# Optimization experiments

Measured on AMD Instinct MI355X. Metric: run time of the kernel, lower is better.

## Reference

```python
import jax, jax.numpy as jnp
import numpy as np

B = 4096           # batch
F = 16             # categorical fields
V = 50000          # vocab per field
D = 128            # embed_dim
T = 2              # task_num
ES = 8             # specific_expert_num
ESH = 8            # shared_expert_num
NUMN = 63          # numerical_num
IN0 = (F + 1) * D  # 2176 = embed_output_dim
H0, H1 = 512, 256  # bottom_mlp_dims
INV = float(1.0 / np.sqrt(1.0 + 1e-5))  # eval BatchNorm1d: running_mean=0, running_var=1


def setup_inputs():
    keys = iter(jax.random.split(jax.random.key(0), 64))
    def nrm(shape, s=0.02):
        return jax.random.normal(next(keys), shape, jnp.float32) * s
    inp = {}
    inp["categorical_x"] = jax.random.randint(next(keys), (B, F), 0, V)
    inp["numerical_x"] = jax.random.normal(next(keys), (B, NUMN), jnp.float32)
    inp["emb_table"] = nrm((F * V, D))
    inp["num_W"] = nrm((NUMN, D)); inp["num_b"] = jnp.zeros((D,), jnp.float32)
    def mlp(prefix, lead, i, o):
        inp[prefix + "_W"] = nrm(lead + (i, o))
        inp[prefix + "_b"] = jnp.zeros(lead + (o,), jnp.float32)
        inp[prefix + "_g"] = jnp.ones(lead + (o,), jnp.float32)    # BN gamma
        inp[prefix + "_be"] = jnp.zeros(lead + (o,), jnp.float32)  # BN beta
    # PLE layer 0 (input dim IN0 -> H0)
    mlp("se0", (ESH,), IN0, H0); mlp("te0", (T, ES), IN0, H0)
    inp["tg0_W"] = nrm((T, IN0, ES + ESH)); inp["tg0_b"] = jnp.zeros((T, ES + ESH), jnp.float32)
    inp["sg0_W"] = nrm((IN0, T * ES + ESH)); inp["sg0_b"] = jnp.zeros((T * ES + ESH,), jnp.float32)
    # PLE layer 1 (H0 -> H1); share gate of last layer is unused in torch forward
    mlp("se1", (ESH,), H0, H1); mlp("te1", (T, ES), H0, H1)
    inp["tg1_W"] = nrm((T, H0, ES + ESH)); inp["tg1_b"] = jnp.zeros((T, ES + ESH), jnp.float32)
    # per-task towers: [H1->128]->BN->ReLU, [128->64]->BN->ReLU, [64->1]
    mlp("tw0", (T,), H1, 128); mlp("tw1", (T,), 128, 64)
    inp["two_W"] = nrm((T, 64, 1)); inp["two_b"] = jnp.zeros((T, 1), jnp.float32)
    return inp


def _ple_layer(shared, tfea, seW, seb, seg, sebe, teW, teb, teg, tebe, tgW, tgb, sgW=None, sgb=None):
    # shared: [B, in]; tfea: [T, B, in]
    nT, nB = tfea.shape[0], tfea.shape[1]
    # shared experts: [B, ESH, o]
    sh = jax.nn.relu((jnp.einsum('bi,eio->beo', shared, seW) + seb) * INV * seg + sebe)
    # task-specific experts: [T, B, ES, o]
    th = jnp.einsum('tbi,teio->tbeo', tfea, teW) + teb[:, None]
    th = jax.nn.relu(th * INV * teg[:, None] + tebe[:, None])
    # per-task gates over [own ES experts ++ shared ESH experts]
    gate = jax.nn.softmax(jnp.einsum('tbi,tig->tbg', tfea, tgW) + tgb[:, None], axis=-1)
    mix = jnp.concatenate([th, jnp.broadcast_to(sh[None], (nT,) + sh.shape)], axis=2)
    new_t = jnp.einsum('tbg,tbgo->tbo', gate, mix)
    if sgW is None:  # last layer: shared branch not updated
        return None, new_t
    # shared gate over [all tasks' experts (task order) ++ shared experts]
    all_mix = jnp.concatenate(
        [jnp.transpose(th, (1, 0, 2, 3)).reshape(nB, nT * th.shape[2], th.shape[3]), sh], axis=1)
    g2 = jax.nn.softmax(shared @ sgW + sgb, axis=-1)
    new_s = jnp.einsum('bg,bgo->bo', g2, all_mix)
    return new_s, new_t


def reference(categorical_x, numerical_x, emb_table, num_W, num_b,
              se0_W, se0_b, se0_g, se0_be, te0_W, te0_b, te0_g, te0_be, tg0_W, tg0_b, sg0_W, sg0_b,
              se1_W, se1_b, se1_g, se1_be, te1_W, te1_b, te1_g, te1_be, tg1_W, tg1_b,
              tw0_W, tw0_b, tw0_g, tw0_be, tw1_W, tw1_b, tw1_g, tw1_be, two_W, two_b):
    offsets = jnp.arange(F) * V
    cat_emb = emb_table[categorical_x + offsets]                         # [B,F,D]
    num_emb = numerical_x @ num_W + num_b                                # [B,D]
    emb = jnp.concatenate([cat_emb.reshape(B, F * D), num_emb], axis=1)  # [B,IN0]
    shared = emb
    tfea = jnp.broadcast_to(emb[None], (T, B, IN0))
    shared, tfea = _ple_layer(shared, tfea, se0_W, se0_b, se0_g, se0_be,
                              te0_W, te0_b, te0_g, te0_be, tg0_W, tg0_b, sg0_W, sg0_b)
    _, tfea = _ple_layer(shared, tfea, se1_W, se1_b, se1_g, se1_be,
                         te1_W, te1_b, te1_g, te1_be, tg1_W, tg1_b)
    # towers (eval BN, dropout identity)
    h = jax.nn.relu((jnp.einsum('tbi,tio->tbo', tfea, tw0_W) + tw0_b[:, None]) * INV * tw0_g[:, None] + tw0_be[:, None])
    h = jax.nn.relu((jnp.einsum('tbi,tio->tbo', h, tw1_W) + tw1_b[:, None]) * INV * tw1_g[:, None] + tw1_be[:, None])
    out = jnp.einsum('tbi,tio->tbo', h, two_W) + two_b[:, None]          # [T,B,1]
    return jax.nn.sigmoid(out[..., 0])                                   # [T,B]
```

## Files before the change

kernel.cpp:

```cpp
#include <hip/hip_runtime.h>

typedef unsigned short u16;
typedef unsigned int u32;
typedef __attribute__((ext_vector_type(4))) u16 u16x4;
typedef __attribute__((ext_vector_type(8))) __bf16 bf16x8;
typedef __attribute__((ext_vector_type(4))) float floatx4;

#define INV_BN 0.9999950000374997f
#define IN0 2176
#define N0EXT 12416
#define N1EXT 2176

__device__ __forceinline__ float b2f(u16 u) {
  return __builtin_bit_cast(float, (u32)u << 16);
}
__device__ __forceinline__ u16 f2b(float f) {
  u32 x = __builtin_bit_cast(u32, f);
  return (u16)((x + 0x7fffu + ((x >> 16) & 1u)) >> 16);
}

__global__ __launch_bounds__(256) void input_build(
    const int* __restrict__ cat, const float* __restrict__ table,
    const float* __restrict__ xn, const float* __restrict__ W,
    const float* __restrict__ bias, u16* __restrict__ X0) {
  int x = blockIdx.x, tid = threadIdx.x;
  if (x < 8192) {
    int idx = x * 256 + tid;
    int d4 = idx & 31;
    int bf = idx >> 5;
    int f = bf & 15;
    int b = bf >> 4;
    long row = (long)cat[bf] + (long)f * 50000;
    float4 v = *((const float4*)(table + row * 128) + d4);
    u16x4 o = {f2b(v.x), f2b(v.y), f2b(v.z), f2b(v.w)};
    *(u16x4*)(X0 + (long)b * IN0 + f * 128 + d4 * 4) = o;
  } else {
    int idx = (x - 8192) * 256 + tid;
    int o = idx & 127;
    int b = idx >> 7;
    float acc = bias[o];
    const float* xr = xn + b * 63;
    for (int k = 0; k < 63; k++) acc = fmaf(xr[k], W[k * 128 + o], acc);
    X0[(long)b * IN0 + 2048 + o] = f2b(acc);
  }
}

__global__ __launch_bounds__(256) void repack_w_all(
    const float* __restrict__ te0W, const float* __restrict__ te0g,
    const float* __restrict__ se0W, const float* __restrict__ se0g,
    const float* __restrict__ te1W, const float* __restrict__ te1g,
    const float* __restrict__ se1W, const float* __restrict__ se1g,
    const float* __restrict__ tw0W, const float* __restrict__ tw0g,
    u16* __restrict__ W0, u16* __restrict__ W1, u16* __restrict__ TW0) {
  int z = blockIdx.z;
  const float *src, *gsc;
  u16* dst;
  int K, O, nBase, e, xm, ym;
  if (z < 16) {
    e = z; src = te0W; gsc = te0g; dst = W0; K = 2176; O = 512; nBase = 0; xm = 68; ym = 16;
  } else if (z < 24) {
    e = z - 16; src = se0W; gsc = se0g; dst = W0; K = 2176; O = 512; nBase = 8192; xm = 68; ym = 16;
  } else if (z < 40) {
    e = z - 24; src = te1W; gsc = te1g; dst = W1; K = 512; O = 256;
    nBase = (e < 8) ? 0 : (N1EXT - 2048); xm = 16; ym = 8;
  } else if (z < 48) {
    e = z - 40; src = se1W; gsc = se1g; dst = W1; K = 512; O = 256; nBase = 2 * N1EXT; xm = 16; ym = 8;
  } else {
    e = z - 48; src = tw0W; gsc = tw0g; dst = TW0; K = 256; O = 128; nBase = 0; xm = 8; ym = 4;
  }
  if (blockIdx.x >= (u32)xm || blockIdx.y >= (u32)ym) return;
  __shared__ float tile[32][33];
  int k0 = blockIdx.x * 32, o0 = blockIdx.y * 32;
  int tx = threadIdx.x & 31, ty = threadIdx.x >> 5;
  const float* S = src + (long)e * K * O;
#pragma unroll
  for (int r = 0; r < 32; r += 8)
    tile[ty + r][tx] = S[(long)(k0 + ty + r) * O + o0 + tx];
  __syncthreads();
#pragma unroll
  for (int r = 0; r < 32; r += 8) {
    int o = o0 + ty + r;
    float s = INV_BN * gsc[e * O + o];
    dst[(long)(nBase + e * O + o) * K + k0 + tx] = f2b(tile[tx][ty + r] * s);
  }
}

__global__ __launch_bounds__(256) void setup_small(
    const float* __restrict__ tg0W, const float* __restrict__ tg0b,
    const float* __restrict__ sg0W, const float* __restrict__ sg0b,
    const float* __restrict__ tg1W, const float* __restrict__ tg1b,
    const float* __restrict__ te0b, const float* __restrict__ te0g, const float* __restrict__ te0be,
    const float* __restrict__ se0b, const float* __restrict__ se0g, const float* __restrict__ se0be,
    const float* __restrict__ te1b, const float* __restrict__ te1g, const float* __restrict__ te1be,
    const float* __restrict__ se1b, const float* __restrict__ se1g, const float* __restrict__ se1be,
    const float* __restrict__ tw0b, const float* __restrict__ tw0g, const float* __restrict__ tw0be,
    const float* __restrict__ tw1W, const float* __restrict__ tw1b,
    const float* __restrict__ tw1g, const float* __restrict__ tw1be,
    u16* __restrict__ W0, u16* __restrict__ W1, u16* __restrict__ TW1,
    float* __restrict__ bias0, float* __restrict__ bias1,
    float* __restrict__ biasT0, float* __restrict__ biasT1) {
  int x = blockIdx.x, tid = threadIdx.x;
  if (x < 128) {
    int g = x;
    u16* dst = W0 + (long)(12288 + g) * IN0;
    for (int k = tid; k < IN0; k += 256) {
      float v;
      if (g < 32) {
        int t = g >> 4, j = g & 15;
        v = tg0W[(long)t * IN0 * 16 + k * 16 + j];
      } else if (g < 56) {
        v = sg0W[k * 24 + (g - 32)];
      } else {
        v = 0.f;
      }
      dst[k] = f2b(v);
    }
    if (tid == 0)
      bias0[12288 + g] = g < 32 ? tg0b[g] : (g < 56 ? sg0b[g - 32] : 0.f);
  } else if (x < 512) {
    int i = x - 128;
    int z = i >> 7, g = i & 127;
    u16* dst = W1 + (long)z * N1EXT * 512 + (long)(2048 + g) * 512;
    for (int k = tid; k < 512; k += 256) {
      float v = (z < 2 && g < 16) ? tg1W[(long)z * 512 * 16 + k * 16 + g] : 0.f;
      dst[k] = f2b(v);
    }
    if (tid == 0)
      bias1[z * N1EXT + 2048 + g] = (z < 2 && g < 16) ? tg1b[z * 16 + g] : 0.f;
  } else if (x < 640) {
    int idx = (x - 512) * 256 + tid;
    int z = idx >> 14, rem = idx & 16383, n = rem >> 7, k = rem & 127;
    float v = 0.f;
    if (n < 64) v = tw1W[(long)z * 128 * 64 + k * 64 + n] * INV_BN * tw1g[z * 64 + n];
    TW1[(long)z * 128 * 128 + n * 128 + k] = f2b(v);
    if (k == 0)
      biasT1[z * 128 + n] =
          (n < 64) ? tw1b[z * 64 + n] * INV_BN * tw1g[z * 64 + n] + tw1be[z * 64 + n] : 0.f;
  } else if (x < 688) {
    int i = (x - 640) * 256 + tid;
    if (i < 8192) bias0[i] = te0b[i] * INV_BN * te0g[i] + te0be[i];
    else {
      int r = i - 8192;
      bias0[i] = se0b[r] * INV_BN * se0g[r] + se0be[r];
    }
  } else if (x < 712) {
    int j = (x - 688) * 256 + tid;
    int z = j >> 11, r = j & 2047;
    float v;
    if (z < 2) v = te1b[z * 2048 + r] * INV_BN * te1g[z * 2048 + r] + te1be[z * 2048 + r];
    else v = se1b[r] * INV_BN * se1g[r] + se1be[r];
    bias1[z * N1EXT + r] = v;
  } else {
    biasT0[tid] = tw0b[tid] * INV_BN * tw0g[tid] + tw0be[tid];
  }
}

__device__ __forceinline__ void gemm_body(
    const u16* __restrict__ A, const u16* __restrict__ Bw, u16* __restrict__ C,
    const float* __restrict__ bias, int N, int K, int reluN, int yOff) {
  __shared__ u16 As[128 * 32];
  __shared__ u16 Bs[128 * 32];
  int tid = threadIdx.x;
  int m0 = blockIdx.x * 128, n0 = (blockIdx.y + yOff) * 128;
  int l = tid & 63, w = tid >> 6;
  int wm = (w >> 1) * 64, wn = (w & 1) * 64;

  const u16* aS0 = A + (long)(m0 + (tid >> 2)) * K + (tid & 3) * 8;
  const u16* aS1 = A + (long)(m0 + 64 + (tid >> 2)) * K + (tid & 3) * 8;
  const u16* bS0 = Bw + (long)(n0 + (tid >> 2)) * K + (tid & 3) * 8;
  const u16* bS1 = Bw + (long)(n0 + 64 + (tid >> 2)) * K + (tid & 3) * 8;
  u16* aD0 = As + tid * 8;
  u16* aD1 = As + (256 + tid) * 8;
  u16* bD0 = Bs + tid * 8;
  u16* bD1 = Bs + (256 + tid) * 8;

  floatx4 acc[4][4] = {};

  int aOff[4], bOff[4];
#pragma unroll
  for (int i = 0; i < 4; i++) {
    aOff[i] = (wm + i * 16 + (l & 15)) * 32 + (l >> 4) * 8;
    bOff[i] = (wn + i * 16 + (l & 15)) * 32 + (l >> 4) * 8;
  }

  for (int k0 = 0; k0 < K; k0 += 32) {
    __builtin_amdgcn_global_load_lds((const __attribute__((address_space(1))) u16*)aS0,
                                     (__attribute__((address_space(3))) u16*)aD0, 16, 0, 0);
    __builtin_amdgcn_global_load_lds((const __attribute__((address_space(1))) u16*)aS1,
                                     (__attribute__((address_space(3))) u16*)aD1, 16, 0, 0);
    __builtin_amdgcn_global_load_lds((const __attribute__((address_space(1))) u16*)bS0,
                                     (__attribute__((address_space(3))) u16*)bD0, 16, 0, 0);
    __builtin_amdgcn_global_load_lds((const __attribute__((address_space(1))) u16*)bS1,
                                     (__attribute__((address_space(3))) u16*)bD1, 16, 0, 0);
    aS0 += 32; aS1 += 32; bS0 += 32; bS1 += 32;
    __syncthreads();
    bf16x8 af[4], bfr[4];
#pragma unroll
    for (int i = 0; i < 4; i++) af[i] = *(const bf16x8*)(As + aOff[i]);
#pragma unroll
    for (int j = 0; j < 4; j++) bfr[j] = *(const bf16x8*)(Bs + bOff[j]);
#pragma unroll
    for (int i = 0; i < 4; i++)
#pragma unroll
      for (int j = 0; j < 4; j++)
        acc[i][j] = __builtin_amdgcn_mfma_f32_16x16x32_bf16(af[i], bfr[j], acc[i][j], 0, 0, 0);
    __syncthreads();
  }

  int cn = n0 + wn + (l & 15);
  int rm = m0 + wm + ((l >> 4) << 2);
#pragma unroll
  for (int j = 0; j < 4; j++) {
    int col = cn + j * 16;
    float bv = bias[col];
    bool doRelu = col < reluN;
#pragma unroll
    for (int i = 0; i < 4; i++)
#pragma unroll
      for (int r = 0; r < 4; r++) {
        float v = acc[i][j][r] + bv;
        v = doRelu ? fmaxf(v, 0.f) : v;
        C[(long)(rm + i * 16 + r) * N + col] = f2b(v);
      }
  }
}

__global__ __launch_bounds__(256) void gemm_l0(
    const u16* __restrict__ A, const u16* __restrict__ Bw, u16* __restrict__ C,
    const float* __restrict__ bias, int yOff) {
  gemm_body(A, Bw, C, bias, N0EXT, IN0, 12288, yOff);
}

__global__ __launch_bounds__(256) void gemm_l1(
    const u16* __restrict__ A, const u16* __restrict__ Bw, u16* __restrict__ C,
    const float* __restrict__ bias) {
  int z = blockIdx.z;
  gemm_body(A + (long)z * 4096 * 512, Bw + (long)z * N1EXT * 512,
            C + (long)z * 4096 * N1EXT, bias + (long)z * N1EXT, N1EXT, 512, 2048, 0);
}

__global__ __launch_bounds__(256) void mix0_kernel(
    const u16* __restrict__ E0, u16* __restrict__ X1) {
  int b = blockIdx.x, tid = threadIdx.x;
  __shared__ float gw[56];
  const u16* row = E0 + (long)b * N0EXT;
  if (tid < 3) {
    int base = (tid == 0) ? 0 : (tid == 1) ? 16 : 32;
    int cnt = (tid == 2) ? 24 : 16;
    const u16* lg = row + 12288 + base;
    float mx = -1e30f;
    for (int i = 0; i < cnt; i++) mx = fmaxf(mx, b2f(lg[i]));
    float sum = 0.f;
    for (int i = 0; i < cnt; i++) {
      float e = __expf(b2f(lg[i]) - mx);
      gw[base + i] = e;
      sum += e;
    }
    float inv = 1.f / sum;
    for (int i = 0; i < cnt; i++) gw[base + i] *= inv;
  }
  __syncthreads();
#pragma unroll
  for (int half = 0; half < 2; half++) {
    int o = tid + half * 256;
    float t0 = 0.f, t1 = 0.f, s = 0.f;
#pragma unroll
    for (int e = 0; e < 8; e++) {
      float v0 = b2f(row[e * 512 + o]);
      float v1 = b2f(row[(8 + e) * 512 + o]);
      float vs = b2f(row[(16 + e) * 512 + o]);
      t0 = fmaf(gw[e], v0, t0);       t0 = fmaf(gw[8 + e], vs, t0);
      t1 = fmaf(gw[16 + e], v1, t1);  t1 = fmaf(gw[24 + e], vs, t1);
      s = fmaf(gw[32 + e], v0, s);
      s = fmaf(gw[40 + e], v1, s);
      s = fmaf(gw[48 + e], vs, s);
    }
    X1[((long)(0 * 4096 + b)) * 512 + o] = f2b(t0);
    X1[((long)(1 * 4096 + b)) * 512 + o] = f2b(t1);
    X1[((long)(2 * 4096 + b)) * 512 + o] = f2b(s);
  }
}

__global__ __launch_bounds__(256) void mix1_kernel(
    const u16* __restrict__ E1, u16* __restrict__ X2) {
  int b = blockIdx.x, tid = threadIdx.x;
  __shared__ float gw[32];
  if (tid < 2) {
    const u16* lg = E1 + ((long)(tid * 4096 + b)) * N1EXT + 2048;
    float mx = -1e30f;
    for (int i = 0; i < 16; i++) mx = fmaxf(mx, b2f(lg[i]));
    float sum = 0.f;
    for (int i = 0; i < 16; i++) {
      float e = __expf(b2f(lg[i]) - mx);
      gw[tid * 16 + i] = e;
      sum += e;
    }
    float inv = 1.f / sum;
    for (int i = 0; i < 16; i++) gw[tid * 16 + i] *= inv;
  }
  __syncthreads();
  int o = tid;
  const u16* r0 = E1 + ((long)(0 * 4096 + b)) * N1EXT;
  const u16* r1 = E1 + ((long)(1 * 4096 + b)) * N1EXT;
  const u16* rs = E1 + ((long)(2 * 4096 + b)) * N1EXT;
  float t0 = 0.f, t1 = 0.f;
#pragma unroll
  for (int e = 0; e < 8; e++) {
    float vs = b2f(rs[e * 256 + o]);
    t0 = fmaf(gw[e], b2f(r0[e * 256 + o]), t0);
    t0 = fmaf(gw[8 + e], vs, t0);
    t1 = fmaf(gw[16 + e], b2f(r1[e * 256 + o]), t1);
    t1 = fmaf(gw[24 + e], vs, t1);
  }
  X2[((long)(0 * 4096 + b)) * 256 + o] = f2b(t0);
  X2[((long)(1 * 4096 + b)) * 256 + o] = f2b(t1);
}

__global__ __launch_bounds__(256) void towers_fused(
    const u16* __restrict__ X2, const u16* __restrict__ TW0,
    const u16* __restrict__ TW1, const float* __restrict__ biasT0,
    const float* __restrict__ biasT1, const float* __restrict__ twoW,
    const float* __restrict__ twob, float* __restrict__ out) {
  __shared__ u16 As[128 * 32];
  __shared__ u16 Bs[128 * 32];
  __shared__ u16 Hs[128 * 136];
  int z = blockIdx.z;
  int tid = threadIdx.x;
  int m0 = blockIdx.x * 128;
  int l = tid & 63, w = tid >> 6;
  int wm = (w >> 1) * 64, wn = (w & 1) * 64;
  int q = l >> 4;

  const u16* A = X2 + (long)z * 4096 * 256;
  const u16* B0 = TW0 + (long)z * 128 * 256;
  const u16* B1 = TW1 + (long)z * 128 * 128;

  int aOff[4], bOff[4];
#pragma unroll
  for (int i = 0; i < 4; i++) {
    aOff[i] = (wm + i * 16 + (l & 15)) * 32 + q * 8;
    bOff[i] = (wn + i * 16 + (l & 15)) * 32 + q * 8;
  }
  int rmLoc = wm + (q << 2);
  int cnLoc = wn + (l & 15);

  {
    const u16* aS0 = A + (long)(m0 + (tid >> 2)) * 256 + (tid & 3) * 8;
    const u16* aS1 = A + (long)(m0 + 64 + (tid >> 2)) * 256 + (tid & 3) * 8;
    const u16* bS0 = B0 + (long)(tid >> 2) * 256 + (tid & 3) * 8;
    const u16* bS1 = B0 + (long)(64 + (tid >> 2)) * 256 + (tid & 3) * 8;
    u16* aD0 = As + tid * 8;
    u16* aD1 = As + (256 + tid) * 8;
    u16* bD0 = Bs + tid * 8;
    u16* bD1 = Bs + (256 + tid) * 8;
    floatx4 acc[4][4] = {};
    for (int k0 = 0; k0 < 256; k0 += 32) {
      __builtin_amdgcn_global_load_lds((const __attribute__((address_space(1))) u16*)aS0,
                                       (__attribute__((address_space(3))) u16*)aD0, 16, 0, 0);
      __builtin_amdgcn_global_load_lds((const __attribute__((address_space(1))) u16*)aS1,
                                       (__attribute__((address_space(3))) u16*)aD1, 16, 0, 0);
      __builtin_amdgcn_global_load_lds((const __attribute__((address_space(1))) u16*)bS0,
                                       (__attribute__((address_space(3))) u16*)bD0, 16, 0, 0);
      __builtin_amdgcn_global_load_lds((const __attribute__((address_space(1))) u16*)bS1,
                                       (__attribute__((address_space(3))) u16*)bD1, 16, 0, 0);
      aS0 += 32; aS1 += 32; bS0 += 32; bS1 += 32;
      __syncthreads();
      bf16x8 af[4], bfr[4];
#pragma unroll
      for (int i = 0; i < 4; i++) af[i] = *(const bf16x8*)(As + aOff[i]);
#pragma unroll
      for (int j = 0; j < 4; j++) bfr[j] = *(const bf16x8*)(Bs + bOff[j]);
#pragma unroll
      for (int i = 0; i < 4; i++)
#pragma unroll
        for (int j = 0; j < 4; j++)
          acc[i][j] = __builtin_amdgcn_mfma_f32_16x16x32_bf16(af[i], bfr[j], acc[i][j], 0, 0, 0);
      __syncthreads();
    }
#pragma unroll
    for (int j = 0; j < 4; j++) {
      int col = cnLoc + j * 16;
      float bv = biasT0[z * 128 + col];
#pragma unroll
      for (int i = 0; i < 4; i++)
#pragma unroll
        for (int r = 0; r < 4; r++)
          Hs[(rmLoc + i * 16 + r) * 136 + col] = f2b(fmaxf(acc[i][j][r] + bv, 0.f));
    }
  }
  __syncthreads();

  floatx4 acc2[4][4] = {};
  {
    const u16* bS0 = B1 + (long)(tid >> 2) * 128 + (tid & 3) * 8;
    const u16* bS1 = B1 + (long)(64 + (tid >> 2)) * 128 + (tid & 3) * 8;
    u16* bD0 = Bs + tid * 8;
    u16* bD1 = Bs + (256 + tid) * 8;
    for (int k0 = 0; k0 < 128; k0 += 32) {
      __builtin_amdgcn_global_load_lds((const __attribute__((address_space(1))) u16*)bS0,
                                       (__attribute__((address_space(3))) u16*)bD0, 16, 0, 0);
      __builtin_amdgcn_global_load_lds((const __attribute__((address_space(1))) u16*)bS1,
                                       (__attribute__((address_space(3))) u16*)bD1, 16, 0, 0);
      bS0 += 32; bS1 += 32;
      __syncthreads();
      bf16x8 af[4], bfr[4];
#pragma unroll
      for (int i = 0; i < 4; i++)
        af[i] = *(const bf16x8*)(Hs + (wm + i * 16 + (l & 15)) * 136 + k0 + q * 8);
#pragma unroll
      for (int j = 0; j < 4; j++) bfr[j] = *(const bf16x8*)(Bs + bOff[j]);
#pragma unroll
      for (int i = 0; i < 4; i++)
#pragma unroll
        for (int j = 0; j < 4; j++)
          acc2[i][j] = __builtin_amdgcn_mfma_f32_16x16x32_bf16(af[i], bfr[j], acc2[i][j], 0, 0, 0);
      __syncthreads();
    }
  }
#pragma unroll
  for (int j = 0; j < 4; j++) {
    int col = cnLoc + j * 16;
    float bv = biasT1[z * 128 + col];
#pragma unroll
    for (int i = 0; i < 4; i++)
#pragma unroll
      for (int r = 0; r < 4; r++)
        Hs[(rmLoc + i * 16 + r) * 136 + col] = f2b(fmaxf(acc2[i][j][r] + bv, 0.f));
  }
  __syncthreads();

  if (tid < 128) {
    const float* wc = twoW + z * 64;
    const u16* xr = Hs + tid * 136;
    float acc = twob[z];
    for (int k = 0; k < 64; k++) acc = fmaf(b2f(xr[k]), wc[k], acc);
    out[z * 4096 + m0 + tid] = 1.f / (1.f + __expf(-acc));
  }
}

extern "C" void kernel_launch(void* const* d_in, const int* in_sizes, int n_in,
                              void* d_out, int out_size, void* d_ws, size_t ws_size,
                              hipStream_t stream) {
  const int* cat = (const int*)d_in[0];
  const float* numx = (const float*)d_in[1];
  const float* table = (const float*)d_in[2];
  const float* numW = (const float*)d_in[3];
  const float* numb = (const float*)d_in[4];
  const float* se0W = (const float*)d_in[5];
  const float* se0b = (const float*)d_in[6];
  const float* se0g = (const float*)d_in[7];
  const float* se0be = (const float*)d_in[8];
  const float* te0W = (const float*)d_in[9];
  const float* te0b = (const float*)d_in[10];
  const float* te0g = (const float*)d_in[11];
  const float* te0be = (const float*)d_in[12];
  const float* tg0W = (const float*)d_in[13];
  const float* tg0b = (const float*)d_in[14];
  const float* sg0W = (const float*)d_in[15];
  const float* sg0b = (const float*)d_in[16];
  const float* se1W = (const float*)d_in[17];
  const float* se1b = (const float*)d_in[18];
  const float* se1g = (const float*)d_in[19];
  const float* se1be = (const float*)d_in[20];
  const float* te1W = (const float*)d_in[21];
  const float* te1b = (const float*)d_in[22];
  const float* te1g = (const float*)d_in[23];
  const float* te1be = (const float*)d_in[24];
  const float* tg1W = (const float*)d_in[25];
  const float* tg1b = (const float*)d_in[26];
  const float* tw0W = (const float*)d_in[27];
  const float* tw0b = (const float*)d_in[28];
  const float* tw0g = (const float*)d_in[29];
  const float* tw0be = (const float*)d_in[30];
  const float* tw1W = (const float*)d_in[31];
  const float* tw1b = (const float*)d_in[32];
  const float* tw1g = (const float*)d_in[33];
  const float* tw1be = (const float*)d_in[34];
  const float* twoW = (const float*)d_in[35];
  const float* twob = (const float*)d_in[36];
  float* out = (float*)d_out;

  char* p = (char*)d_ws;
  u16* X0 = (u16*)p;        p += (size_t)4096 * IN0 * 2;
  u16* W0 = (u16*)p;        p += (size_t)N0EXT * IN0 * 2;
  float* bias0 = (float*)p; p += (size_t)N0EXT * 4;
  u16* X1 = (u16*)p;        p += (size_t)3 * 4096 * 512 * 2;
  u16* W1 = (u16*)p;        p += (size_t)3 * N1EXT * 512 * 2;
  float* bias1 = (float*)p; p += (size_t)3 * N1EXT * 4;
  u16* X2 = (u16*)p;        p += (size_t)2 * 4096 * 256 * 2;
  u16* TW0 = (u16*)p;       p += (size_t)2 * 128 * 256 * 2;
  float* biasT0 = (float*)p; p += (size_t)256 * 4;
  u16* TW1 = (u16*)p;       p += (size_t)2 * 128 * 128 * 2;
  float* biasT1 = (float*)p; p += (size_t)256 * 4;
  u16* E0 = (u16*)p;
  u16* E1 = (u16*)p;

  input_build<<<10240, 256, 0, stream>>>(cat, table, numx, numW, numb, X0);
  repack_w_all<<<dim3(68, 16, 50), 256, 0, stream>>>(
      te0W, te0g, se0W, se0g, te1W, te1g, se1W, se1g, tw0W, tw0g, W0, W1, TW0);
  setup_small<<<713, 256, 0, stream>>>(
      tg0W, tg0b, sg0W, sg0b, tg1W, tg1b,
      te0b, te0g, te0be, se0b, se0g, se0be,
      te1b, te1g, te1be, se1b, se1g, se1be,
      tw0b, tw0g, tw0be, tw1W, tw1b, tw1g, tw1be,
      W0, W1, TW1, bias0, bias1, biasT0, biasT1);

  gemm_l0<<<dim3(32, 49), 256, 0, stream>>>(X0, W0, E0, bias0, 0);
  gemm_l0<<<dim3(32, 48), 256, 0, stream>>>(X0, W0, E0, bias0, 49);
  mix0_kernel<<<4096, 256, 0, stream>>>(E0, X1);

  gemm_l1<<<dim3(32, 17, 3), 256, 0, stream>>>(X1, W1, E1, bias1);
  mix1_kernel<<<4096, 256, 0, stream>>>(E1, X2);

  towers_fused<<<dim3(32, 1, 2), 256, 0, stream>>>(
      X2, TW0, TW1, biasT0, biasT1, twoW, twob, out);
}
```

Measured before the change: 981.5 us.

## Add 256x256-tile 8-wave GEMM with direct global-to-LDS pipelined loads

```diff
diff --git a/kernel.cpp b/kernel.cpp
--- a/kernel.cpp
+++ b/kernel.cpp
@@ -233,10 +233,156 @@
 
 __global__ __launch_bounds__(256) void gemm_l1(
     const u16* __restrict__ A, const u16* __restrict__ Bw, u16* __restrict__ C,
+    const float* __restrict__ bias, int yOff) {
+  int z = blockIdx.z;
+  gemm_body(A + (long)z * 4096 * 512, Bw + (long)z * N1EXT * 512,
+            C + (long)z * 4096 * N1EXT, bias + (long)z * N1EXT, N1EXT, 512, 2048, yOff);
+}
+
+#define GL_LDS(SRC, DST)                                                              \
+  __builtin_amdgcn_global_load_lds((const __attribute__((address_space(1))) u16*)(SRC), \
+                                   (__attribute__((address_space(3))) u16*)(DST), 16, 0, 0)
+#define STG(PTR, DOFF)                     \
+  do {                                     \
+    GL_LDS((PTR), L + (DOFF) + tid * 8);   \
+    (PTR) += 64;                           \
+  } while (0)
+#define FEN asm volatile("" ::: "memory")
+#define BARR                        \
+  do {                              \
+    FEN;                            \
+    __builtin_amdgcn_s_barrier();   \
+    FEN;                            \
+  } while (0)
+#define VMW(N) asm volatile("s_waitcnt vmcnt(" #N ")" ::: "memory")
+
+#define RD_A(BB, MH)                                                                      \
+  _Pragma("unroll") for (int i = 0; i < 4; i++) {                                         \
+    af[i][0] = *(const bf16x8*)(Lb + (BB) * 32768 + aFB + ((MH) * 4 + i) * 2048 + sp0);   \
+    af[i][1] = *(const bf16x8*)(Lb + (BB) * 32768 + aFB + ((MH) * 4 + i) * 2048 + sp1);   \
+  }
+#define RD_B(BB, NH, ARR)                                                                 \
+  _Pragma("unroll") for (int j = 0; j < 2; j++) {                                         \
+    ARR[j][0] = *(const bf16x8*)(Lb + (BB) * 32768 + bFB + ((NH) * 2 + j) * 2048 + sp0);  \
+    ARR[j][1] = *(const bf16x8*)(Lb + (BB) * 32768 + bFB + ((NH) * 2 + j) * 2048 + sp1);  \
+  }
+#define MMA(MH, NH, ARR)                                                                  \
+  __builtin_amdgcn_s_setprio(1);                                                          \
+  _Pragma("unroll") for (int i = 0; i < 4; i++)                                           \
+  _Pragma("unroll") for (int j = 0; j < 2; j++) {                                         \
+    acc[(MH) * 4 + i][(NH) * 2 + j] = __builtin_amdgcn_mfma_f32_16x16x32_bf16(            \
+        af[i][0], ARR[j][0], acc[(MH) * 4 + i][(NH) * 2 + j], 0, 0, 0);                   \
+    acc[(MH) * 4 + i][(NH) * 2 + j] = __builtin_amdgcn_mfma_f32_16x16x32_bf16(            \
+        af[i][1], ARR[j][1], acc[(MH) * 4 + i][(NH) * 2 + j], 0, 0, 0);                   \
+  }                                                                                       \
+  __builtin_amdgcn_s_setprio(0)
+
+template <bool FULL>
+__device__ __forceinline__ void giter8(
+    u16* L, const char* Lb, int tid,
+    const u16* (&sAp)[2][2], const u16* (&sBp)[2][2],
+    bf16x8 (&af)[4][2], bf16x8 (&bf0)[2][2], bf16x8 (&bf1)[2][2],
+    floatx4 (&acc)[8][4], int aFB, int bFB, int sp0, int sp1) {
+  RD_A(0, 0); RD_B(0, 0, bf0);
+  STG(sAp[0][1], 20480); STG(sAp[1][1], 28672);
+  BARR; MMA(0, 0, bf0); BARR;
+  RD_B(0, 1, bf1);
+  STG(sBp[0][0], 49152); STG(sBp[1][0], 57344);
+  BARR; MMA(0, 1, bf1); BARR;
+  RD_A(0, 1);
+  STG(sBp[0][1], 53248); STG(sBp[1][1], 61440);
+  BARR; MMA(1, 1, bf1); BARR;
+  if constexpr (FULL) { STG(sAp[0][0], 0); STG(sAp[1][0], 8192); }
+  BARR; MMA(1, 0, bf0);
+  if constexpr (FULL) { VMW(2); } else { VMW(0); }
+  BARR;
+  RD_A(1, 0); RD_B(1, 0, bf0);
+  if constexpr (FULL) { STG(sBp[0][0], 32768); STG(sBp[1][0], 40960); }
+  BARR; MMA(0, 0, bf0); BARR;
+  RD_B(1, 1, bf1);
+  if constexpr (FULL) { STG(sBp[0][1], 36864); STG(sBp[1][1], 45056); }
+  BARR; MMA(0, 1, bf1); BARR;
+  RD_A(1, 1);
+  if constexpr (FULL) { STG(sAp[0][1], 4096); STG(sAp[1][1], 12288); }
+  BARR; MMA(1, 1, bf1); BARR;
+  if constexpr (FULL) { STG(sAp[0][0], 16384); STG(sAp[1][0], 24576); }
+  BARR; MMA(1, 0, bf0);
+  if constexpr (FULL) { VMW(2); }
+  BARR;
+}
+
+__device__ __forceinline__ void gemm256_body(
+    const u16* __restrict__ A, const u16* __restrict__ Bw, u16* __restrict__ C,
+    const float* __restrict__ bias, const int K, const int N, const int NIT) {
+  __shared__ u16 L[65536];
+  const int tid = threadIdx.x;
+  const int l = tid & 63, w = tid >> 6;
+  const int wr = w >> 2, wc = w & 3;
+  const int rl = l & 15;
+  const int m0 = blockIdx.x * 256, n0 = blockIdx.y * 256;
+
+  const int srow = tid >> 3;
+  const long stgOff = (long)srow * K + (((tid & 7) ^ (srow & 7)) * 8);
+  const u16* sAp[2][2];
+  const u16* sBp[2][2];
+#pragma unroll
+  for (int h = 0; h < 2; h++)
+#pragma unroll
+    for (int rb = 0; rb < 2; rb++) {
+      sAp[h][rb] = A + (long)(m0 + h * 128 + rb * 64) * K + stgOff;
+      sBp[h][rb] = Bw + (long)(n0 + h * 128 + rb * 64) * K + stgOff;
+    }
+
+  STG(sAp[0][0], 0);     STG(sAp[1][0], 8192);
+  STG(sAp[0][1], 4096);  STG(sAp[1][1], 12288);
+  STG(sBp[0][0], 32768); STG(sBp[1][0], 40960);
+  STG(sBp[0][1], 36864); STG(sBp[1][1], 45056);
+  STG(sAp[0][0], 16384); STG(sAp[1][0], 24576);
+
+  const char* Lb = (const char*)L;
+  const int aFB = wr * 16384 + rl * 128;
+  const int bFB = 65536 + (wc >> 1) * 16384 + (wc & 1) * 8192 + rl * 128;
+  const int sp0 = ((l >> 4) ^ (l & 7)) * 16;
+  const int sp1 = (((l >> 4) + 4) ^ (l & 7)) * 16;
+
+  floatx4 acc[8][4] = {};
+  bf16x8 af[4][2], bf0[2][2], bf1[2][2];
+
+  VMW(2);
+  BARR;
+
+  for (int it = 0; it < NIT - 1; ++it)
+    giter8<true>(L, Lb, tid, sAp, sBp, af, bf0, bf1, acc, aFB, bFB, sp0, sp1);
+  giter8<false>(L, Lb, tid, sAp, sBp, af, bf0, bf1, acc, aFB, bFB, sp0, sp1);
+
+  const int colB = n0 + wc * 64 + rl;
+  const int rowB = m0 + wr * 128 + (l >> 4) * 4;
+#pragma unroll
+  for (int j = 0; j < 4; j++) {
+    int col = colB + j * 16;
+    float bv = bias[col];
+#pragma unroll
+    for (int i = 0; i < 8; i++)
+#pragma unroll
+      for (int r = 0; r < 4; r++) {
+        float v = fmaxf(acc[i][j][r] + bv, 0.f);
+        C[(long)(rowB + i * 16 + r) * N + col] = f2b(v);
+      }
+  }
+}
+
+__global__ __launch_bounds__(512, 2) void gemm_l0_256(
+    const u16* __restrict__ A, const u16* __restrict__ Bw, u16* __restrict__ C,
+    const float* __restrict__ bias) {
+  gemm256_body(A, Bw, C, bias, 2176, N0EXT, 17);
+}
+
+__global__ __launch_bounds__(512, 2) void gemm_l1_256(
+    const u16* __restrict__ A, const u16* __restrict__ Bw, u16* __restrict__ C,
     const float* __restrict__ bias) {
   int z = blockIdx.z;
-  gemm_body(A + (long)z * 4096 * 512, Bw + (long)z * N1EXT * 512,
-            C + (long)z * 4096 * N1EXT, bias + (long)z * N1EXT, N1EXT, 512, 2048, 0);
+  gemm256_body(A + (long)z * 4096 * 512, Bw + (long)z * N1EXT * 512,
+               C + (long)z * 4096 * N1EXT, bias + (long)z * N1EXT, 512, N1EXT, 4);
 }
 
 __global__ __launch_bounds__(256) void mix0_kernel(
@@ -505,11 +651,12 @@
       tw0b, tw0g, tw0be, tw1W, tw1b, tw1g, tw1be,
       W0, W1, TW1, bias0, bias1, biasT0, biasT1);
 
-  gemm_l0<<<dim3(32, 49), 256, 0, stream>>>(X0, W0, E0, bias0, 0);
-  gemm_l0<<<dim3(32, 48), 256, 0, stream>>>(X0, W0, E0, bias0, 49);
+  gemm_l0_256<<<dim3(16, 48), 512, 0, stream>>>(X0, W0, E0, bias0);
+  gemm_l0<<<dim3(32, 1), 256, 0, stream>>>(X0, W0, E0, bias0, 96);
   mix0_kernel<<<4096, 256, 0, stream>>>(E0, X1);
 
-  gemm_l1<<<dim3(32, 17, 3), 256, 0, stream>>>(X1, W1, E1, bias1);
+  gemm_l1_256<<<dim3(16, 8, 3), 512, 0, stream>>>(X1, W1, E1, bias1);
+  gemm_l1<<<dim3(32, 1, 3), 256, 0, stream>>>(X1, W1, E1, bias1, 16);
   mix1_kernel<<<4096, 256, 0, stream>>>(E1, X2);
 
   towers_fused<<<dim3(32, 1, 2), 256, 0, stream>>>(
```

Result: faster. 950.0 us (-3.2%).
